# Performance work log

Hardware: AMD Instinct MI355X
Metric: run time of the kernel (lower is better)

The kernel has to match this reference:

```python
import jax, jax.numpy as jnp
import numpy as np


def setup_inputs() -> dict:
    key = jax.random.key(0)
    ks = jax.random.split(key, 5)
    B, S, D, O = 8, 2048, 1024, 1024
    q = jax.random.normal(ks[0], (B, S, D), dtype=jnp.float32)
    k = jax.random.normal(ks[1], (B, S, D), dtype=jnp.float32)
    # glorot-scale weights
    scale = (2.0 / (D + O)) ** 0.5
    Wq = jax.random.normal(ks[2], (D, O), dtype=jnp.float32) * scale
    Wk = jax.random.normal(ks[3], (D, O), dtype=jnp.float32) * scale
    Wv = jax.random.normal(ks[4], (D, O), dtype=jnp.float32) * scale
    return {"q": q, "k": k, "Wq": Wq, "Wk": Wk, "Wv": Wv}


def reference(q, k, Wq, Wk, Wv):
    # q: [B, S, Dq], k: [B, S, Dk]
    q_proj = jnp.einsum('bsd,do->bso', q, Wq)   # [B, S, O]
    k_proj = jnp.einsum('bsd,do->bso', k, Wk)   # [B, S, O]
    v_proj = jnp.einsum('bsd,do->bso', k, Wv)   # [B, S, O]
    # Dot(axes=-1): contract feature dims -> [B, Sq, Sk]; NO 1/sqrt(d) scaling
    attn = jnp.einsum('bqo,bko->bqk', q_proj, k_proj)
    attn_w = jax.nn.softmax(attn, axis=-1)      # softmax over key axis
    # Dot(axes=1): contracts the QUERY axis of attn with the seq axis of v (attn^T @ v)
    context = jnp.einsum('bqk,bqo->bko', attn_w, v_proj)  # [B, S, O]
    return jnp.concatenate([q, context], axis=-1)  # [B, S, Dq + O]
```

## Files before the change

kernel.cpp:

```cpp
#include <hip/hip_runtime.h>
#include <hip/hip_bf16.h>


typedef __attribute__((ext_vector_type(4))) float f32x4;
typedef __attribute__((ext_vector_type(16))) float f32x16;
typedef _Float16 f16;
typedef __attribute__((ext_vector_type(8))) _Float16 f16x8;
typedef __attribute__((ext_vector_type(4))) _Float16 f16x4;

#define LOG2E 1.4426950408889634f

#define CM_F32     0
#define CM_F16     1
#define CM_F16T    3
#define CM_ATTN    4
#define CM_PROJ2   5
#define CM_PVS     6

#define STAGE(WHICH, KS, KT, BO) do { \
    const char* _gb = (WHICH) ? Bb : Ab; \
    const int _ld = (WHICH) ? ldb : lda; \
    const long _r = (WHICH) ? (long)(bn + srow0) : (long)(bm + srow0); \
    const int _k0 = (KT) * 64 + (KS) * 32 + sh8; \
    char* _dst = (char*)smem + (BO) + (WHICH) * 32768 + (KS) * 16384 + wave * 1024; \
    const char* _g0 = _gb + ((_r * _ld + _k0) << 1); \
    const char* _g1 = _gb + (((_r + 128) * _ld + _k0) << 1); \
    __builtin_amdgcn_global_load_lds((const __attribute__((address_space(1))) void*)_g0, \
        (__attribute__((address_space(3))) void*)_dst, 16, 0, 0); \
    __builtin_amdgcn_global_load_lds((const __attribute__((address_space(1))) void*)_g1, \
        (__attribute__((address_space(3))) void*)(_dst + 8192), 16, 0, 0); \
} while (0)

#define GPHASE2(KS, STAGE_CODE, VM) do { \
    f16x8 af[2][4], bb[2][2], sv[2]; \
    _Pragma("unroll") \
    for (int s = 0; s < 2; ++s) { \
        _Pragma("unroll") \
        for (int mt = 0; mt < 4; ++mt) \
            af[s][mt] = *(const f16x8*)(smem + \
                ((bufo + (KS) * 16384 + abase[mt]) ^ (s << 5))); \
        _Pragma("unroll") \
        for (int nt = 0; nt < 2; ++nt) \
            bb[s][nt] = *(const f16x8*)(smem + \
                ((bufo + (KS) * 16384 + bbase[nt]) ^ (s << 5))); \
        if (CMODE == CM_PVS) \
            sv[s] = *(const f16x8*)(smem + 131072 + wm * 4096 + \
                t * 128 + (KS) * 64 + s * 32 + (h5 << 4)); \
    } \
    if (CMODE == CM_PVS) { \
        _Pragma("unroll") \
        for (int s = 0; s < 2; ++s) \
            _Pragma("unroll") \
            for (int mt = 0; mt < 4; ++mt) \
                af[s][mt] *= sv[s]; \
    } \
    __builtin_amdgcn_s_barrier(); \
    __builtin_amdgcn_s_setprio(1); \
    STAGE_CODE; \
    _Pragma("unroll") \
    for (int s = 0; s < 2; ++s) \
        _Pragma("unroll") \
        for (int mt = 0; mt < 4; ++mt) \
            _Pragma("unroll") \
            for (int nt = 0; nt < 2; ++nt) \
                acc[mt][nt] = __builtin_amdgcn_mfma_f32_32x32x16_f16( \
                    af[s][mt], bb[s][nt], acc[mt][nt], 0, 0, 0); \
    __builtin_amdgcn_s_setprio(0); \
    VM; \
    __builtin_amdgcn_s_barrier(); \
} while (0)

template<int CMODE>
__global__ __launch_bounds__(512, 2)
void gemm256(const f16* __restrict__ A, const f16* __restrict__ B,
             void* __restrict__ Cv,
             int M, int N, int K, int lda, int ldb, int ldc,
             long az, long bz, long cz,
             float* __restrict__ pm, float* __restrict__ ps)
{
    __shared__ __align__(16) char smem[139264];

    const int z = blockIdx.z;
    const char* Ab;
    const char* Bb;
    if (CMODE == CM_PROJ2) {
        const int y = blockIdx.y;
        Ab = (const char*)(A + (y ? (long)M * 1024 : 0));
        Bb = (const char*)(B + (long)y * 1024 * 1024);
    } else {
        Ab = (const char*)(A + z * az);
        Bb = (const char*)(B + z * bz);
    }

    const int nbx = N >> 8;
    int wg = blockIdx.x;
    const int nwg = gridDim.x;
    if ((nwg & 7) == 0) wg = (wg & 7) * (nwg >> 3) + (wg >> 3);
    const int bm = (wg / nbx) << 8;
    const int bn = (wg % nbx) << 8;

    const int tid = threadIdx.x;
    const int wave = tid >> 6;
    const int lane = tid & 63;
    const int l31 = lane & 31;
    const int h5 = lane >> 5;
    const int wm = wave >> 2;
    const int wn = wave & 3;

    const int f3 = (l31 ^ (l31 >> 2)) & 3;
    const int sl = ((h5 ^ f3) << 4);
    int abase[4], bbase[2];
    #pragma unroll
    for (int mt = 0; mt < 4; ++mt)
        abase[mt] = (wm * 128 + mt * 32 + l31) * 64 + sl;
    #pragma unroll
    for (int nt = 0; nt < 2; ++nt)
        bbase[nt] = 32768 + (wn * 64 + nt * 32 + l31) * 64 + sl;

    const int srow0 = tid >> 2;
    const int sh8 = ((tid ^ (tid >> 2) ^ (tid >> 4)) & 3) * 8;

    f32x16 acc[4][2];
    #pragma unroll
    for (int mt = 0; mt < 4; ++mt)
        #pragma unroll
        for (int nt = 0; nt < 2; ++nt)
            acc[mt][nt] = (f32x16)(0.f);

    const int nt_k = K >> 6;

    {
        if (CMODE == CM_PVS) {
            const char* gsc = (const char*)ps +
                (((long)z * 16 + (bm >> 7)) * 2048) * 2 + tid * 16;
            __builtin_amdgcn_global_load_lds(
                (const __attribute__((address_space(1))) void*)gsc,
                (__attribute__((address_space(3))) void*)
                    ((char*)smem + 131072 + wave * 1024), 16, 0, 0);
        }
        const int t1p = (nt_k > 1) ? 1 : 0;
        STAGE(0, 0, 0, 0);
        STAGE(1, 0, 0, 0);
        STAGE(0, 1, 0, 0);
        STAGE(1, 1, 0, 0);
        STAGE(0, 0, t1p, 65536);
        STAGE(1, 0, t1p, 65536);
        asm volatile("s_waitcnt vmcnt(4)" ::: "memory");
        __builtin_amdgcn_s_barrier();
    }

    for (int t = 0; t < nt_k; ++t) {
        const int bufo = (t & 1) << 16;
        const int nbo = bufo ^ 65536;
        const int t1 = (t + 1 < nt_k) ? t + 1 : nt_k - 1;
        const int t2 = (t + 2 < nt_k) ? t + 2 : nt_k - 1;
        GPHASE2(0, { STAGE(0, 1, t1, nbo); STAGE(1, 1, t1, nbo); }, );
        GPHASE2(1, { STAGE(0, 0, t2, bufo); STAGE(1, 0, t2, bufo); },
                asm volatile("s_waitcnt vmcnt(4)" ::: "memory"));
    }
    asm volatile("s_waitcnt vmcnt(0)" ::: "memory");

    if (CMODE == CM_ATTN) {
        f16* E = (f16*)Cv + z * cz;
        #pragma unroll
        for (int nt = 0; nt < 2; ++nt) {
            float Mx = -3.4e38f;
            #pragma unroll
            for (int mt = 0; mt < 4; ++mt)
                #pragma unroll
                for (int r = 0; r < 16; ++r)
                    Mx = fmaxf(Mx, acc[mt][nt][r]);
            Mx = fmaxf(Mx, __shfl_xor(Mx, 32, 64));
            float Sm = 0.f;
            #pragma unroll
            for (int mt = 0; mt < 4; ++mt)
                #pragma unroll
                for (int r = 0; r < 16; ++r) {
                    const float e = exp2f((acc[mt][nt][r] - Mx) * LOG2E);
                    acc[mt][nt][r] = e;
                    Sm += e;
                }
            Sm += __shfl_xor(Sm, 32, 64);
            const int col = bn + wn * 64 + nt * 32 + l31;
            #pragma unroll
            for (int mt = 0; mt < 4; ++mt) {
                const int row0 = bm + wm * 128 + mt * 32 + h5 * 4;
                #pragma unroll
                for (int rq = 0; rq < 4; ++rq)
                    #pragma unroll
                    for (int rr = 0; rr < 4; ++rr)
                        E[(long)(row0 + rq * 8 + rr) * ldc + col] =
                            (f16)acc[mt][nt][rq * 4 + rr];
            }
            if (lane < 32) {
                const long pidx = ((long)z * 16 + (bm >> 7) + wm) * N + col;
                pm[pidx] = Mx * LOG2E;
                ps[pidx] = Sm;
            }
        }
        return;
    }

    #pragma unroll
    for (int mt = 0; mt < 4; ++mt) {
        #pragma unroll
        for (int nt = 0; nt < 2; ++nt) {
            const int row0 = bm + wm * 128 + mt * 32 + h5 * 4;
            const int col = bn + wn * 64 + nt * 32 + l31;
            if (CMODE == CM_F32 || CMODE == CM_PVS) {
                float* C = (float*)Cv + z * cz;
                #pragma unroll
                for (int rq = 0; rq < 4; ++rq)
                    #pragma unroll
                    for (int rr = 0; rr < 4; ++rr)
                        C[(long)(row0 + rq * 8 + rr) * ldc + col] =
                            acc[mt][nt][rq * 4 + rr];
            } else if (CMODE == CM_F16) {
                f16* C = (f16*)Cv + z * cz;
                #pragma unroll
                for (int rq = 0; rq < 4; ++rq)
                    #pragma unroll
                    for (int rr = 0; rr < 4; ++rr)
                        C[(long)(row0 + rq * 8 + rr) * ldc + col] =
                            (f16)acc[mt][nt][rq * 4 + rr];
            } else if (CMODE == CM_F16T) {
                f16* C = (f16*)Cv + z * cz;
                #pragma unroll
                for (int rq = 0; rq < 4; ++rq) {
                    f16x4 v;
                    #pragma unroll
                    for (int rr = 0; rr < 4; ++rr) v[rr] = (f16)acc[mt][nt][rq * 4 + rr];
                    *(f16x4*)(C + (long)col * ldc + row0 + rq * 8) = v;
                }
            } else {
                const int y = blockIdx.y;
                if (y == 0) {
                    f16* C = (f16*)Cv;
                    #pragma unroll
                    for (int rq = 0; rq < 4; ++rq)
                        #pragma unroll
                        for (int rr = 0; rr < 4; ++rr)
                            C[(long)(row0 + rq * 8 + rr) * 1024 + col] =
                                (f16)acc[mt][nt][rq * 4 + rr];
                } else {
                    f16* C = (f16*)pm;
                    #pragma unroll
                    for (int rq = 0; rq < 4; ++rq) {
                        f16x4 v;
                        #pragma unroll
                        for (int rr = 0; rr < 4; ++rr)
                            v[rr] = (f16)acc[mt][nt][rq * 4 + rr];
                        *(f16x4*)(C + (long)col * M + row0 + rq * 8) = v;
                    }
                }
            }
        }
    }
}

__global__ __launch_bounds__(256)
void pack_cast_qk(const float* __restrict__ qin, const float* __restrict__ kin,
                  f16* __restrict__ qp, f16* __restrict__ kp,
                  float* __restrict__ oq, long nquads)
{
    const long i = (long)blockIdx.x * 256 + threadIdx.x;
    if (i >= 2 * nquads) return;
    const int isK = (i >= nquads);
    const long j = isK ? i - nquads : i;
    const long row = j >> 8;
    const int c = (int)(j & 255) * 4;
    const float4 v = isK ? *(const float4*)(kin + row * 1024 + c)
                         : *(const float4*)(qin + row * 1024 + c);
    f16x4 h;
    h[0] = (f16)v.x; h[1] = (f16)v.y; h[2] = (f16)v.z; h[3] = (f16)v.w;
    if (isK) {
        *(f16x4*)(kp + row * 1024 + c) = h;
    } else {
        *(float4*)(oq + row * 2048 + c) = v;
        *(f16x4*)(qp + row * 1024 + c) = h;
    }
}

__global__ __launch_bounds__(256)
void cast_f16(const float* __restrict__ in, f16* __restrict__ outp, long nquads)
{
    const long i = (long)blockIdx.x * 256 + threadIdx.x;
    if (i >= nquads) return;
    const long row = i >> 8;
    const int c = (int)(i & 255) * 4;
    const float4 v = *(const float4*)(in + row * 1024 + c);
    f16x4 h;
    h[0] = (f16)v.x; h[1] = (f16)v.y; h[2] = (f16)v.z; h[3] = (f16)v.w;
    *(f16x4*)(outp + row * 1024 + c) = h;
}

__global__ __launch_bounds__(256)
void pack_W_T(const float* __restrict__ W, f16* __restrict__ Wt)
{
    __shared__ float tile[64][65];
    const int d0 = blockIdx.y * 64, o0 = blockIdx.x * 64;
    const int t = threadIdx.x;
    const int rr = t >> 4, c4 = (t & 15) * 4;
    #pragma unroll
    for (int it = 0; it < 4; ++it) {
        const int r = rr + it * 16;
        const float4 v = *(const float4*)(W + (long)(d0 + r) * 1024 + o0 + c4);
        tile[r][c4] = v.x; tile[r][c4 + 1] = v.y;
        tile[r][c4 + 2] = v.z; tile[r][c4 + 3] = v.w;
    }
    __syncthreads();
    #pragma unroll
    for (int it = 0; it < 4; ++it) {
        const int orow = rr + it * 16;
        f16x4 h;
        #pragma unroll
        for (int j = 0; j < 4; ++j) h[j] = (f16)tile[c4 + j][orow];
        *(f16x4*)(Wt + (long)(o0 + orow) * 1024 + d0 + c4) = h;
    }
}

__global__ __launch_bounds__(256)
void gt_reduce(const float* __restrict__ P, f16* __restrict__ Gt, long nquads)
{
    const long i = (long)blockIdx.x * 256 + threadIdx.x;
    if (i >= nquads) return;
    float4 s = *(const float4*)(P + i * 4);
    #pragma unroll
    for (int z = 1; z < 8; ++z) {
        const float4 v = *(const float4*)(P + (long)z * 1048576 + i * 4);
        s.x += v.x; s.y += v.y; s.z += v.z; s.w += v.w;
    }
    f16x4 h;
    h[0] = (f16)s.x; h[1] = (f16)s.y; h[2] = (f16)s.z; h[3] = (f16)s.w;
    *(f16x4*)(Gt + i * 4) = h;
}

__global__ __launch_bounds__(256)
void softmax_merge16(const float* __restrict__ pm, const float* __restrict__ ps,
                     f16* __restrict__ scale, int nq)
{
    const int idx = blockIdx.x * 256 + threadIdx.x;
    if (idx >= nq) return;
    const int z = idx >> 11, q = idx & 2047;
    const float* pmz = pm + ((long)z * 16) * 2048 + q;
    const float* psz = ps + ((long)z * 16) * 2048 + q;
    float mx = -3.4e38f;
    #pragma unroll
    for (int j = 0; j < 16; ++j) mx = fmaxf(mx, pmz[j * 2048]);
    float s = 0.f;
    #pragma unroll
    for (int j = 0; j < 16; ++j)
        s += psz[j * 2048] * exp2f(pmz[j * 2048] - mx);
    const float L = mx + log2f(s);
    f16* sc = scale + ((long)z * 16) * 2048 + q;
    #pragma unroll
    for (int j = 0; j < 16; ++j)
        sc[j * 2048] = (f16)exp2f(pmz[j * 2048] - L);
}

__global__ __launch_bounds__(256)
void copy_q_kernel(const float* __restrict__ q, float* __restrict__ out, long n4)
{
    const long idx = (long)blockIdx.x * 256 + threadIdx.x;
    if (idx >= n4) return;
    const long row = idx >> 8;
    const long c4 = idx & 255;
    *(float4*)(&out[row * 2048 + c4 * 4]) =
        *(const float4*)(&q[row * 1024 + c4 * 4]);
}

#define BM 64
#define BN 64
#define BKF 16
template<int opA, int opB>
__global__ __launch_bounds__(256)
void sgemm(const float* __restrict__ A, const float* __restrict__ B,
           float* __restrict__ C,
           int M, int N, int K, int lda, int ldb, int ldc)
{
    __shared__ float As[BKF][BM];
    __shared__ float Bs[BKF][BN];
    const int tid = threadIdx.x;
    const int tx = tid & 15, ty = tid >> 4;
    const int bm = blockIdx.y * BM, bn = blockIdx.x * BN;
    float acc[4][4] = {};
    for (int k0 = 0; k0 < K; k0 += BKF) {
        if (opA == 0) {
            const int row = tid >> 2, kq = (tid & 3) * 4;
            const float4 v = *(const float4*)(A + (long)(bm + row) * lda + (k0 + kq));
            As[kq + 0][row] = v.x; As[kq + 1][row] = v.y;
            As[kq + 2][row] = v.z; As[kq + 3][row] = v.w;
        } else {
            const int kk = tid >> 4, mq = (tid & 15) * 4;
            *(float4*)(&As[kk][mq]) =
                *(const float4*)(A + (long)(k0 + kk) * lda + (bm + mq));
        }
        if (opB == 0) {
            const int kk = tid >> 4, nq = (tid & 15) * 4;
            *(float4*)(&Bs[kk][nq]) =
                *(const float4*)(B + (long)(k0 + kk) * ldb + (bn + nq));
        } else {
            const int row = tid >> 2, kq = (tid & 3) * 4;
            const float4 v = *(const float4*)(B + (long)(bn + row) * ldb + (k0 + kq));
            Bs[kq + 0][row] = v.x; Bs[kq + 1][row] = v.y;
            Bs[kq + 2][row] = v.z; Bs[kq + 3][row] = v.w;
        }
        __syncthreads();
        #pragma unroll
        for (int kk = 0; kk < BKF; ++kk) {
            const float4 a = *(const float4*)(&As[kk][ty * 4]);
            const float4 b = *(const float4*)(&Bs[kk][tx * 4]);
            const float av[4] = {a.x, a.y, a.z, a.w};
            const float bv[4] = {b.x, b.y, b.z, b.w};
            #pragma unroll
            for (int i = 0; i < 4; ++i)
                #pragma unroll
                for (int j = 0; j < 4; ++j)
                    acc[i][j] += av[i] * bv[j];
        }
        __syncthreads();
    }
    #pragma unroll
    for (int i = 0; i < 4; ++i) {
        const float4 v = make_float4(acc[i][0], acc[i][1], acc[i][2], acc[i][3]);
        *(float4*)(&C[(long)(bm + ty * 4 + i) * ldc + (bn + tx * 4)]) = v;
    }
}

__device__ __forceinline__ float wave_reduce_max(float v) {
    #pragma unroll
    for (int off = 1; off < 64; off <<= 1)
        v = fmaxf(v, __shfl_xor(v, off, 64));
    return v;
}
__device__ __forceinline__ float wave_reduce_sum(float v) {
    #pragma unroll
    for (int off = 1; off < 64; off <<= 1)
        v += __shfl_xor(v, off, 64);
    return v;
}

__global__ __launch_bounds__(256)
void softmax_rows2048(float* __restrict__ X)
{
    float* x = X + (long)blockIdx.x * 2048;
    const int tid = threadIdx.x;
    float4 v0 = *(const float4*)(&x[tid * 4]);
    float4 v1 = *(const float4*)(&x[1024 + tid * 4]);
    float m = fmaxf(fmaxf(fmaxf(v0.x, v0.y), fmaxf(v0.z, v0.w)),
                    fmaxf(fmaxf(v1.x, v1.y), fmaxf(v1.z, v1.w)));
    m = wave_reduce_max(m);
    __shared__ float sm[4];
    __shared__ float ss[4];
    const int wid = tid >> 6;
    if ((tid & 63) == 0) sm[wid] = m;
    __syncthreads();
    m = fmaxf(fmaxf(sm[0], sm[1]), fmaxf(sm[2], sm[3]));
    v0.x = expf(v0.x - m); v0.y = expf(v0.y - m);
    v0.z = expf(v0.z - m); v0.w = expf(v0.w - m);
    v1.x = expf(v1.x - m); v1.y = expf(v1.y - m);
    v1.z = expf(v1.z - m); v1.w = expf(v1.w - m);
    float s = (v0.x + v0.y + v0.z + v0.w) + (v1.x + v1.y + v1.z + v1.w);
    s = wave_reduce_sum(s);
    if ((tid & 63) == 0) ss[wid] = s;
    __syncthreads();
    s = ss[0] + ss[1] + ss[2] + ss[3];
    const float inv = 1.0f / s;
    v0.x *= inv; v0.y *= inv; v0.z *= inv; v0.w *= inv;
    v1.x *= inv; v1.y *= inv; v1.z *= inv; v1.w *= inv;
    *(float4*)(&x[tid * 4]) = v0;
    *(float4*)(&x[1024 + tid * 4]) = v1;
}

static void fallback_fp32(const float* q, const float* k, const float* Wq,
                          const float* Wk, const float* Wv, float* out,
                          void* d_ws, hipStream_t stream)
{
    const int S = 2048, D = 1024, O = 1024, B = 8;
    float* qp = (float*)d_ws;
    float* kp = qp + (size_t)S * O;
    float* vp = kp + (size_t)S * O;
    float* attn = vp + (size_t)S * O;
    const long n4 = (long)B * S * D / 4;
    copy_q_kernel<<<dim3((n4 + 255) / 256), 256, 0, stream>>>(q, out, n4);
    const dim3 blk(256);
    const dim3 gproj(O / BN, S / BM), gattn(S / BN, S / BM), gctx(O / BN, S / BM);
    for (int b = 0; b < B; ++b) {
        const float* qb = q + (size_t)b * S * D;
        const float* kb = k + (size_t)b * S * D;
        float* outc = out + (size_t)b * S * 2048 + D;
        sgemm<0, 0><<<gproj, blk, 0, stream>>>(qb, Wq, qp, S, O, D, D, O, O);
        sgemm<0, 0><<<gproj, blk, 0, stream>>>(kb, Wk, kp, S, O, D, D, O, O);
        sgemm<0, 0><<<gproj, blk, 0, stream>>>(kb, Wv, vp, S, O, D, D, O, O);
        sgemm<0, 1><<<gattn, blk, 0, stream>>>(qp, kp, attn, S, S, O, O, O, S);
        softmax_rows2048<<<dim3(S), blk, 0, stream>>>(attn);
        sgemm<1, 0><<<gctx, blk, 0, stream>>>(attn, vp, outc, S, O, S, S, O, 2048);
    }
}

extern "C" void kernel_launch(void* const* d_in, const int* in_sizes, int n_in,
                              void* d_out, int out_size, void* d_ws, size_t ws_size,
                              hipStream_t stream)
{
    const float* q  = (const float*)d_in[0];
    const float* k  = (const float*)d_in[1];
    const float* Wq = (const float*)d_in[2];
    const float* Wk = (const float*)d_in[3];
    const float* Wv = (const float*)d_in[4];
    float* out = (float*)d_out;

    const int B = 8, S = 2048;

    auto need = [](int g) -> size_t {
        const size_t fixed = ((size_t)1024 * 1024 * 2) * 4
                           + (size_t)8 * 1024 * 1024 * 4;
        const size_t pkA = (size_t)g * 2048 * 1024 * 2;
        const size_t vpT = (size_t)1024 * g * 2048 * 2;
        const size_t aw  = (size_t)g * 2048 * 2048 * 2;
        const size_t pp  = 2 * (size_t)g * 16 * 2048 * 4 + (size_t)g * 16 * 2048 * 2;
        return fixed + 3 * pkA + vpT + aw + pp + 32 * 256;
    };
    int g = 0;
    for (int cand : {8, 4, 2, 1})
        if (need(cand) <= ws_size) { g = cand; break; }
    if (g == 0) { fallback_fp32(q, k, Wq, Wk, Wv, out, d_ws, stream); return; }

    char* p = (char*)d_ws;
    auto carve = [&](size_t bytes) {
        char* r = p;
        p += (bytes + 255) & ~(size_t)255;
        return r;
    };
    f16* Gt   = (f16*)carve((size_t)1024 * 1024 * 2);
    f16* Wtv  = (f16*)carve((size_t)1024 * 1024 * 2);
    f16* Wq_h = (f16*)carve((size_t)1024 * 1024 * 2);
    f16* Wk_h = (f16*)carve((size_t)1024 * 1024 * 2);
    float* Gp = (float*)carve((size_t)8 * 1024 * 1024 * 4);
    const size_t pkAB = (size_t)g * 2048 * 1024 * 2;
    f16* qpack  = (f16*)carve(pkAB);
    f16* kpack  = (f16*)carve(pkAB);
    f16* qG     = (f16*)carve(pkAB);
    f16* vpT    = (f16*)carve((size_t)1024 * g * 2048 * 2);
    f16* attn_w = (f16*)carve((size_t)g * 2048 * 2048 * 2);
    float* pmb  = (float*)carve((size_t)g * 16 * 2048 * 4);
    float* psb  = (float*)carve((size_t)g * 16 * 2048 * 4);
    f16* scb    = (f16*)carve((size_t)g * 16 * 2048 * 2);

    const dim3 blk(256);
    const dim3 blk512(512);

    pack_W_T<<<dim3(16, 16), blk, 0, stream>>>(Wv, Wtv);
    cast_f16<<<dim3(1024), blk, 0, stream>>>(Wq, Wq_h, 1024 * 256);
    cast_f16<<<dim3(1024), blk, 0, stream>>>(Wk, Wk_h, 1024 * 256);
    gemm256<CM_F32><<<dim3(16, 1, 8), blk512, 0, stream>>>(
        Wk_h, Wq_h, Gp, 1024, 1024, 128, 1024, 1024, 1024,
        128, 128, (long)1024 * 1024, nullptr, nullptr);
    gt_reduce<<<dim3(1024), blk, 0, stream>>>(Gp, Gt, 1024 * 256);

    const int Mg = g * 2048;
    const long zSS = (long)2048 * 2048;
    const long zSD = (long)2048 * 1024;

    for (int gi = 0; gi < B / g; ++gi) {
        const float* qg = q + (size_t)gi * Mg * 1024;
        const float* kg = k + (size_t)gi * Mg * 1024;
        float* outq = out + (size_t)gi * Mg * 2048;

        const long nquads = (long)Mg * 256;
        pack_cast_qk<<<dim3((2 * nquads + 255) / 256), blk, 0, stream>>>(
            qg, kg, qpack, kpack, outq, nquads);

        const dim3 g1((1024 / 256) * (Mg / 256), 2, 1);
        gemm256<CM_PROJ2><<<g1, blk512, 0, stream>>>(
            qpack, Gt, qG, Mg, 1024, 1024, 1024, 1024, 1024, 0, 0, 0,
            (float*)vpT, nullptr);

        const dim3 g2((2048 / 256) * (2048 / 256), 1, g);
        gemm256<CM_ATTN><<<g2, blk512, 0, stream>>>(
            kpack, qG, attn_w, 2048, 2048, 1024, 1024, 1024, 2048,
            zSD, zSD, zSS, pmb, psb);

        const int nq = g * 2048;
        softmax_merge16<<<dim3((nq + 255) / 256), blk, 0, stream>>>(pmb, psb, scb, nq);

        float* outg = out + (size_t)gi * Mg * 2048 + 1024;
        const dim3 g3((1024 / 256) * (2048 / 256), 1, g);
        gemm256<CM_PVS><<<g3, blk512, 0, stream>>>(
            attn_w, vpT, outg, 2048, 1024, 2048, 2048, Mg, 2048,
            zSS, 2048, zSS, nullptr, (float*)scb);
    }
}
```

Before: 348.1 us.

## Replace pipelined 256x256 GEMM with simple single-buffered 128x128 tile kernel

Swaps the 512-thread, 256x256-tile, double-buffered GEMM (32x32x16 MFMA, swizzled LDS, software pipelining) for a 256-thread 128x128-tile kernel with 16x16x32 MFMA, a single LDS buffer and two barriers per K step of 32. Softmax partials now come in 32 row blocks instead of 16, so the merge kernel and buffers grow to match. This raises the block count and lowers LDS use per block, but it drops the load/compute overlap, halves data reuse per tile, and the unswizzled LDS layout may cause bank conflicts.

```diff
diff --git a/kernel.cpp b/kernel.cpp
--- a/kernel.cpp
+++ b/kernel.cpp
@@ -3,7 +3,6 @@
 
 
 typedef __attribute__((ext_vector_type(4))) float f32x4;
-typedef __attribute__((ext_vector_type(16))) float f32x16;
 typedef _Float16 f16;
 typedef __attribute__((ext_vector_type(8))) _Float16 f16x8;
 typedef __attribute__((ext_vector_type(4))) _Float16 f16x4;
@@ -12,73 +11,27 @@
 
 #define CM_F32     0
 #define CM_F16     1
-#define CM_F16T    3
 #define CM_ATTN    4
 #define CM_PROJ2   5
 #define CM_PVS     6
 
-#define STAGE(WHICH, KS, KT, BO) do { \
-    const char* _gb = (WHICH) ? Bb : Ab; \
-    const int _ld = (WHICH) ? ldb : lda; \
-    const long _r = (WHICH) ? (long)(bn + srow0) : (long)(bm + srow0); \
-    const int _k0 = (KT) * 64 + (KS) * 32 + sh8; \
-    char* _dst = (char*)smem + (BO) + (WHICH) * 32768 + (KS) * 16384 + wave * 1024; \
-    const char* _g0 = _gb + ((_r * _ld + _k0) << 1); \
-    const char* _g1 = _gb + (((_r + 128) * _ld + _k0) << 1); \
-    __builtin_amdgcn_global_load_lds((const __attribute__((address_space(1))) void*)_g0, \
-        (__attribute__((address_space(3))) void*)_dst, 16, 0, 0); \
-    __builtin_amdgcn_global_load_lds((const __attribute__((address_space(1))) void*)_g1, \
-        (__attribute__((address_space(3))) void*)(_dst + 8192), 16, 0, 0); \
-} while (0)
-
-#define GPHASE2(KS, STAGE_CODE, VM) do { \
-    f16x8 af[2][4], bb[2][2], sv[2]; \
-    _Pragma("unroll") \
-    for (int s = 0; s < 2; ++s) { \
-        _Pragma("unroll") \
-        for (int mt = 0; mt < 4; ++mt) \
-            af[s][mt] = *(const f16x8*)(smem + \
-                ((bufo + (KS) * 16384 + abase[mt]) ^ (s << 5))); \
-        _Pragma("unroll") \
-        for (int nt = 0; nt < 2; ++nt) \
-            bb[s][nt] = *(const f16x8*)(smem + \
-                ((bufo + (KS) * 16384 + bbase[nt]) ^ (s << 5))); \
-        if (CMODE == CM_PVS) \
-            sv[s] = *(const f16x8*)(smem + 131072 + wm * 4096 + \
-                t * 128 + (KS) * 64 + s * 32 + (h5 << 4)); \
-    } \
-    if (CMODE == CM_PVS) { \
-        _Pragma("unroll") \
-        for (int s = 0; s < 2; ++s) \
-            _Pragma("unroll") \
-            for (int mt = 0; mt < 4; ++mt) \
-                af[s][mt] *= sv[s]; \
-    } \
-    __builtin_amdgcn_s_barrier(); \
-    __builtin_amdgcn_s_setprio(1); \
-    STAGE_CODE; \
-    _Pragma("unroll") \
-    for (int s = 0; s < 2; ++s) \
-        _Pragma("unroll") \
-        for (int mt = 0; mt < 4; ++mt) \
-            _Pragma("unroll") \
-            for (int nt = 0; nt < 2; ++nt) \
-                acc[mt][nt] = __builtin_amdgcn_mfma_f32_32x32x16_f16( \
-                    af[s][mt], bb[s][nt], acc[mt][nt], 0, 0, 0); \
-    __builtin_amdgcn_s_setprio(0); \
-    VM; \
-    __builtin_amdgcn_s_barrier(); \
-} while (0)
+#define GLD(SRC, DST) \
+    __builtin_amdgcn_global_load_lds( \
+        (const __attribute__((address_space(1))) void*)(SRC), \
+        (__attribute__((address_space(3))) void*)(DST), 16, 0, 0)
 
 template<int CMODE>
-__global__ __launch_bounds__(512, 2)
-void gemm256(const f16* __restrict__ A, const f16* __restrict__ B,
+__global__ __launch_bounds__(256)
+void gemm128(const f16* __restrict__ A, const f16* __restrict__ B,
              void* __restrict__ Cv,
              int M, int N, int K, int lda, int ldb, int ldc,
              long az, long bz, long cz,
              float* __restrict__ pm, float* __restrict__ ps)
 {
-    __shared__ __align__(16) char smem[139264];
+    __shared__ __align__(16) char smem[24576];
+    f16* As = (f16*)smem;
+    f16* Bs = (f16*)(smem + 8192);
+    f16* Sc = (f16*)(smem + 16384);
 
     const int z = blockIdx.z;
     const char* Ab;
@@ -92,108 +45,105 @@
         Bb = (const char*)(B + z * bz);
     }
 
-    const int nbx = N >> 8;
+    const int nbx = N >> 7;
     int wg = blockIdx.x;
     const int nwg = gridDim.x;
     if ((nwg & 7) == 0) wg = (wg & 7) * (nwg >> 3) + (wg >> 3);
-    const int bm = (wg / nbx) << 8;
-    const int bn = (wg % nbx) << 8;
+    const int bm = (wg / nbx) << 7;
+    const int bn = (wg % nbx) << 7;
 
     const int tid = threadIdx.x;
     const int wave = tid >> 6;
     const int lane = tid & 63;
-    const int l31 = lane & 31;
-    const int h5 = lane >> 5;
-    const int wm = wave >> 2;
-    const int wn = wave & 3;
-
-    const int f3 = (l31 ^ (l31 >> 2)) & 3;
-    const int sl = ((h5 ^ f3) << 4);
-    int abase[4], bbase[2];
+    const int r16 = lane & 15;
+    const int h4 = lane >> 4;
+    const int wm = wave >> 1;
+    const int wn = wave & 1;
+
+    const int srow = tid >> 2;
+    const int skc = (tid & 3) * 8;
+
+    f32x4 acc[4][4];
     #pragma unroll
     for (int mt = 0; mt < 4; ++mt)
-        abase[mt] = (wm * 128 + mt * 32 + l31) * 64 + sl;
-    #pragma unroll
-    for (int nt = 0; nt < 2; ++nt)
-        bbase[nt] = 32768 + (wn * 64 + nt * 32 + l31) * 64 + sl;
-
-    const int srow0 = tid >> 2;
-    const int sh8 = ((tid ^ (tid >> 2) ^ (tid >> 4)) & 3) * 8;
-
-    f32x16 acc[4][2];
-    #pragma unroll
-    for (int mt = 0; mt < 4; ++mt)
-        #pragma unroll
-        for (int nt = 0; nt < 2; ++nt)
-            acc[mt][nt] = (f32x16)(0.f);
-
-    const int nt_k = K >> 6;
-
-    {
+        #pragma unroll
+        for (int nt = 0; nt < 4; ++nt)
+            acc[mt][nt] = f32x4{0.f, 0.f, 0.f, 0.f};
+
+    if (CMODE == CM_PVS) {
+        const char* gsc = (const char*)ps +
+            (((long)z * 32 + (bm >> 6)) * 2048) * 2 + lane * 16;
+        GLD(gsc + wave * 1024, (char*)smem + 16384 + wave * 1024);
+        GLD(gsc + 4096 + wave * 1024, (char*)smem + 20480 + wave * 1024);
+    }
+
+    const int ntk = K >> 5;
+    for (int t = 0; t < ntk; ++t) {
+        __syncthreads();
+        const int k0 = t * 32 + skc;
+        GLD(Ab + ((long)(bm + srow) * lda + k0) * 2,
+            (char*)smem + wave * 1024);
+        GLD(Ab + ((long)(bm + 64 + srow) * lda + k0) * 2,
+            (char*)smem + 4096 + wave * 1024);
+        GLD(Bb + ((long)(bn + srow) * ldb + k0) * 2,
+            (char*)smem + 8192 + wave * 1024);
+        GLD(Bb + ((long)(bn + 64 + srow) * ldb + k0) * 2,
+            (char*)smem + 12288 + wave * 1024);
+        __syncthreads();
+
+        f16x8 a4[4], b4[4];
+        #pragma unroll
+        for (int mt = 0; mt < 4; ++mt)
+            a4[mt] = *(const f16x8*)(As + (wm * 64 + mt * 16 + r16) * 32 + h4 * 8);
+        #pragma unroll
+        for (int nt = 0; nt < 4; ++nt)
+            b4[nt] = *(const f16x8*)(Bs + (wn * 64 + nt * 16 + r16) * 32 + h4 * 8);
         if (CMODE == CM_PVS) {
-            const char* gsc = (const char*)ps +
-                (((long)z * 16 + (bm >> 7)) * 2048) * 2 + tid * 16;
-            __builtin_amdgcn_global_load_lds(
-                (const __attribute__((address_space(1))) void*)gsc,
-                (__attribute__((address_space(3))) void*)
-                    ((char*)smem + 131072 + wave * 1024), 16, 0, 0);
+            const f16x8 sv = *(const f16x8*)(Sc + wm * 2048 + t * 32 + h4 * 8);
+            #pragma unroll
+            for (int mt = 0; mt < 4; ++mt) a4[mt] *= sv;
         }
-        const int t1p = (nt_k > 1) ? 1 : 0;
-        STAGE(0, 0, 0, 0);
-        STAGE(1, 0, 0, 0);
-        STAGE(0, 1, 0, 0);
-        STAGE(1, 1, 0, 0);
-        STAGE(0, 0, t1p, 65536);
-        STAGE(1, 0, t1p, 65536);
-        asm volatile("s_waitcnt vmcnt(4)" ::: "memory");
-        __builtin_amdgcn_s_barrier();
-    }
-
-    for (int t = 0; t < nt_k; ++t) {
-        const int bufo = (t & 1) << 16;
-        const int nbo = bufo ^ 65536;
-        const int t1 = (t + 1 < nt_k) ? t + 1 : nt_k - 1;
-        const int t2 = (t + 2 < nt_k) ? t + 2 : nt_k - 1;
-        GPHASE2(0, { STAGE(0, 1, t1, nbo); STAGE(1, 1, t1, nbo); }, );
-        GPHASE2(1, { STAGE(0, 0, t2, bufo); STAGE(1, 0, t2, bufo); },
-                asm volatile("s_waitcnt vmcnt(4)" ::: "memory"));
-    }
-    asm volatile("s_waitcnt vmcnt(0)" ::: "memory");
+        #pragma unroll
+        for (int mt = 0; mt < 4; ++mt)
+            #pragma unroll
+            for (int nt = 0; nt < 4; ++nt)
+                acc[mt][nt] = __builtin_amdgcn_mfma_f32_16x16x32_f16(
+                    a4[mt], b4[nt], acc[mt][nt], 0, 0, 0);
+    }
 
     if (CMODE == CM_ATTN) {
         f16* E = (f16*)Cv + z * cz;
         #pragma unroll
-        for (int nt = 0; nt < 2; ++nt) {
+        for (int nt = 0; nt < 4; ++nt) {
             float Mx = -3.4e38f;
             #pragma unroll
             for (int mt = 0; mt < 4; ++mt)
                 #pragma unroll
-                for (int r = 0; r < 16; ++r)
+                for (int r = 0; r < 4; ++r)
                     Mx = fmaxf(Mx, acc[mt][nt][r]);
+            Mx = fmaxf(Mx, __shfl_xor(Mx, 16, 64));
             Mx = fmaxf(Mx, __shfl_xor(Mx, 32, 64));
             float Sm = 0.f;
             #pragma unroll
             for (int mt = 0; mt < 4; ++mt)
                 #pragma unroll
-                for (int r = 0; r < 16; ++r) {
+                for (int r = 0; r < 4; ++r) {
                     const float e = exp2f((acc[mt][nt][r] - Mx) * LOG2E);
                     acc[mt][nt][r] = e;
                     Sm += e;
                 }
+            Sm += __shfl_xor(Sm, 16, 64);
             Sm += __shfl_xor(Sm, 32, 64);
-            const int col = bn + wn * 64 + nt * 32 + l31;
+            const int col = bn + wn * 64 + nt * 16 + r16;
             #pragma unroll
             for (int mt = 0; mt < 4; ++mt) {
-                const int row0 = bm + wm * 128 + mt * 32 + h5 * 4;
+                const int row0 = bm + wm * 64 + mt * 16 + h4 * 4;
                 #pragma unroll
-                for (int rq = 0; rq < 4; ++rq)
-                    #pragma unroll
-                    for (int rr = 0; rr < 4; ++rr)
-                        E[(long)(row0 + rq * 8 + rr) * ldc + col] =
-                            (f16)acc[mt][nt][rq * 4 + rr];
+                for (int r = 0; r < 4; ++r)
+                    E[(long)(row0 + r) * ldc + col] = (f16)acc[mt][nt][r];
             }
-            if (lane < 32) {
-                const long pidx = ((long)z * 16 + (bm >> 7) + wm) * N + col;
+            if (lane < 16) {
+                const long pidx = ((long)z * 32 + (bm >> 6) + wm) * N + col;
                 pm[pidx] = Mx * LOG2E;
                 ps[pidx] = Sm;
             }
@@ -204,54 +154,31 @@
     #pragma unroll
     for (int mt = 0; mt < 4; ++mt) {
         #pragma unroll
-        for (int nt = 0; nt < 2; ++nt) {
-            const int row0 = bm + wm * 128 + mt * 32 + h5 * 4;
-            const int col = bn + wn * 64 + nt * 32 + l31;
+        for (int nt = 0; nt < 4; ++nt) {
+            const int row0 = bm + wm * 64 + mt * 16 + h4 * 4;
+            const int col = bn + wn * 64 + nt * 16 + r16;
             if (CMODE == CM_F32 || CMODE == CM_PVS) {
                 float* C = (float*)Cv + z * cz;
                 #pragma unroll
-                for (int rq = 0; rq < 4; ++rq)
-                    #pragma unroll
-                    for (int rr = 0; rr < 4; ++rr)
-                        C[(long)(row0 + rq * 8 + rr) * ldc + col] =
-                            acc[mt][nt][rq * 4 + rr];
+                for (int r = 0; r < 4; ++r)
+                    C[(long)(row0 + r) * ldc + col] = acc[mt][nt][r];
             } else if (CMODE == CM_F16) {
                 f16* C = (f16*)Cv + z * cz;
                 #pragma unroll
-                for (int rq = 0; rq < 4; ++rq)
+                for (int r = 0; r < 4; ++r)
+                    C[(long)(row0 + r) * ldc + col] = (f16)acc[mt][nt][r];
+            } else {
+                if (blockIdx.y == 0) {
+                    f16* C = (f16*)Cv;
                     #pragma unroll
-                    for (int rr = 0; rr < 4; ++rr)
-                        C[(long)(row0 + rq * 8 + rr) * ldc + col] =
-                            (f16)acc[mt][nt][rq * 4 + rr];
-            } else if (CMODE == CM_F16T) {
-                f16* C = (f16*)Cv + z * cz;
-                #pragma unroll
-                for (int rq = 0; rq < 4; ++rq) {
+                    for (int r = 0; r < 4; ++r)
+                        C[(long)(row0 + r) * 1024 + col] = (f16)acc[mt][nt][r];
+                } else {
+                    f16* C = (f16*)pm;
                     f16x4 v;
                     #pragma unroll
-                    for (int rr = 0; rr < 4; ++rr) v[rr] = (f16)acc[mt][nt][rq * 4 + rr];
-                    *(f16x4*)(C + (long)col * ldc + row0 + rq * 8) = v;
-                }
-            } else {
-                const int y = blockIdx.y;
-                if (y == 0) {
-                    f16* C = (f16*)Cv;
-                    #pragma unroll
-                    for (int rq = 0; rq < 4; ++rq)
-                        #pragma unroll
-                        for (int rr = 0; rr < 4; ++rr)
-                            C[(long)(row0 + rq * 8 + rr) * 1024 + col] =
-                                (f16)acc[mt][nt][rq * 4 + rr];
-                } else {
-                    f16* C = (f16*)pm;
-                    #pragma unroll
-                    for (int rq = 0; rq < 4; ++rq) {
-                        f16x4 v;
-                        #pragma unroll
-                        for (int rr = 0; rr < 4; ++rr)
-                            v[rr] = (f16)acc[mt][nt][rq * 4 + rr];
-                        *(f16x4*)(C + (long)col * M + row0 + rq * 8) = v;
-                    }
+                    for (int r = 0; r < 4; ++r) v[r] = (f16)acc[mt][nt][r];
+                    *(f16x4*)(C + (long)col * M + row0) = v;
                 }
             }
         }
@@ -336,25 +263,25 @@
 }
 
 __global__ __launch_bounds__(256)
-void softmax_merge16(const float* __restrict__ pm, const float* __restrict__ ps,
+void softmax_merge32(const float* __restrict__ pm, const float* __restrict__ ps,
                      f16* __restrict__ scale, int nq)
 {
     const int idx = blockIdx.x * 256 + threadIdx.x;
     if (idx >= nq) return;
     const int z = idx >> 11, q = idx & 2047;
-    const float* pmz = pm + ((long)z * 16) * 2048 + q;
-    const float* psz = ps + ((long)z * 16) * 2048 + q;
+    const float* pmz = pm + ((long)z * 32) * 2048 + q;
+    const float* psz = ps + ((long)z * 32) * 2048 + q;
     float mx = -3.4e38f;
     #pragma unroll
-    for (int j = 0; j < 16; ++j) mx = fmaxf(mx, pmz[j * 2048]);
+    for (int j = 0; j < 32; ++j) mx = fmaxf(mx, pmz[j * 2048]);
     float s = 0.f;
     #pragma unroll
-    for (int j = 0; j < 16; ++j)
+    for (int j = 0; j < 32; ++j)
         s += psz[j * 2048] * exp2f(pmz[j * 2048] - mx);
     const float L = mx + log2f(s);
-    f16* sc = scale + ((long)z * 16) * 2048 + q;
-    #pragma unroll
-    for (int j = 0; j < 16; ++j)
+    f16* sc = scale + ((long)z * 32) * 2048 + q;
+    #pragma unroll
+    for (int j = 0; j < 32; ++j)
         sc[j * 2048] = (f16)exp2f(pmz[j * 2048] - L);
 }
 
@@ -517,7 +444,7 @@
         const size_t pkA = (size_t)g * 2048 * 1024 * 2;
         const size_t vpT = (size_t)1024 * g * 2048 * 2;
         const size_t aw  = (size_t)g * 2048 * 2048 * 2;
-        const size_t pp  = 2 * (size_t)g * 16 * 2048 * 4 + (size_t)g * 16 * 2048 * 2;
+        const size_t pp  = 2 * (size_t)g * 32 * 2048 * 4 + (size_t)g * 32 * 2048 * 2;
         return fixed + 3 * pkA + vpT + aw + pp + 32 * 256;
     };
     int g = 0;
@@ -542,17 +469,16 @@
     f16* qG     = (f16*)carve(pkAB);
     f16* vpT    = (f16*)carve((size_t)1024 * g * 2048 * 2);
     f16* attn_w = (f16*)carve((size_t)g * 2048 * 2048 * 2);
-    float* pmb  = (float*)carve((size_t)g * 16 * 2048 * 4);
-    float* psb  = (float*)carve((size_t)g * 16 * 2048 * 4);
-    f16* scb    = (f16*)carve((size_t)g * 16 * 2048 * 2);
+    float* pmb  = (float*)carve((size_t)g * 32 * 2048 * 4);
+    float* psb  = (float*)carve((size_t)g * 32 * 2048 * 4);
+    f16* scb    = (f16*)carve((size_t)g * 32 * 2048 * 2);
 
     const dim3 blk(256);
-    const dim3 blk512(512);
 
     pack_W_T<<<dim3(16, 16), blk, 0, stream>>>(Wv, Wtv);
     cast_f16<<<dim3(1024), blk, 0, stream>>>(Wq, Wq_h, 1024 * 256);
     cast_f16<<<dim3(1024), blk, 0, stream>>>(Wk, Wk_h, 1024 * 256);
-    gemm256<CM_F32><<<dim3(16, 1, 8), blk512, 0, stream>>>(
+    gemm128<CM_F32><<<dim3(64, 1, 8), blk, 0, stream>>>(
         Wk_h, Wq_h, Gp, 1024, 1024, 128, 1024, 1024, 1024,
         128, 128, (long)1024 * 1024, nullptr, nullptr);
     gt_reduce<<<dim3(1024), blk, 0, stream>>>(Gp, Gt, 1024 * 256);
@@ -570,22 +496,22 @@
         pack_cast_qk<<<dim3((2 * nquads + 255) / 256), blk, 0, stream>>>(
             qg, kg, qpack, kpack, outq, nquads);
 
-        const dim3 g1((1024 / 256) * (Mg / 256), 2, 1);
-        gemm256<CM_PROJ2><<<g1, blk512, 0, stream>>>(
+        const dim3 g1((1024 / 128) * (Mg / 128), 2, 1);
+        gemm128<CM_PROJ2><<<g1, blk, 0, stream>>>(
             qpack, Gt, qG, Mg, 1024, 1024, 1024, 1024, 1024, 0, 0, 0,
             (float*)vpT, nullptr);
 
-        const dim3 g2((2048 / 256) * (2048 / 256), 1, g);
-        gemm256<CM_ATTN><<<g2, blk512, 0, stream>>>(
+        const dim3 g2((2048 / 128) * (2048 / 128), 1, g);
+        gemm128<CM_ATTN><<<g2, blk, 0, stream>>>(
             kpack, qG, attn_w, 2048, 2048, 1024, 1024, 1024, 2048,
             zSD, zSD, zSS, pmb, psb);
 
         const int nq = g * 2048;
-        softmax_merge16<<<dim3((nq + 255) / 256), blk, 0, stream>>>(pmb, psb, scb, nq);
+        softmax_merge32<<<dim3((nq + 255) / 256), blk, 0, stream>>>(pmb, psb, scb, nq);
 
         float* outg = out + (size_t)gi * Mg * 2048 + 1024;
-        const dim3 g3((1024 / 256) * (2048 / 256), 1, g);
-        gemm256<CM_PVS><<<g3, blk512, 0, stream>>>(
+        const dim3 g3((1024 / 128) * (2048 / 128), 1, g);
+        gemm128<CM_PVS><<<g3, blk, 0, stream>>>(
             attn_w, vpT, outg, 2048, 1024, 2048, 2048, Mg, 2048,
             zSS, 2048, zSS, nullptr, (float*)scb);
     }
```

Measured after the change: 423.3 us. +21.6%, slower.
